# Kernel optimization log

Measured on AMD Instinct MI355X. Metric: run time of the kernel, lower is better.

The kernel has to match this reference:

```python
import jax, jax.numpy as jnp
import numpy as np
import math

B, N, E, F_IN, H = 16, 2048, 32768, 32, 128
RATIO = 0.8
K1 = math.ceil(RATIO * N)      # 1639
K2 = math.ceil(RATIO * K1)     # 1312
K3 = math.ceil(RATIO * K2)     # 1050


def setup_inputs() -> dict:
    key = jax.random.key(0)
    ks = jax.random.split(key, 20)

    def lin(k, out_d, in_d):
        s = 1.0 / np.sqrt(in_d)
        return jax.random.uniform(k, (out_d, in_d), minval=-s, maxval=s, dtype=jnp.float32)

    return {
        "x": jax.random.normal(ks[0], (B, N, F_IN), dtype=jnp.float32),
        "edge_index": jax.random.randint(ks[1], (B, 2, E), 0, N, dtype=jnp.int32),
        "W_root1": lin(ks[2], H, F_IN), "W_rel1": lin(ks[3], H, F_IN), "b1": jnp.zeros((H,), jnp.float32),
        "p1": jax.random.normal(ks[4], (H,), dtype=jnp.float32) * 0.1,
        "W_root2": lin(ks[5], H, H), "W_rel2": lin(ks[6], H, H), "b2": jnp.zeros((H,), jnp.float32),
        "p2": jax.random.normal(ks[7], (H,), dtype=jnp.float32) * 0.1,
        "W_root3": lin(ks[8], H, H), "W_rel3": lin(ks[9], H, H), "b3": jnp.zeros((H,), jnp.float32),
        "p3": jax.random.normal(ks[10], (H,), dtype=jnp.float32) * 0.1,
        "lin1_W": lin(ks[11], 128, 256), "lin1_b": jnp.zeros((128,), jnp.float32),
        "lin2_W": lin(ks[12], 64, 128), "lin2_b": jnp.zeros((64,), jnp.float32),
        "lin3_W": lin(ks[13], 1, 64), "lin3_b": jnp.zeros((1,), jnp.float32),
    }


def _graph_conv(x, src, dst, ev, W_rel, b, W_root):
    # GraphConv: out_i = W_root x_i + W_rel * sum_{j->i} x_j + b
    n = x.shape[0]
    msg = x[src] * ev[:, None].astype(x.dtype)            # [E, F] gather
    agg = jnp.zeros((n, x.shape[1]), x.dtype).at[dst].add(msg)  # scatter-add
    return agg @ W_rel.T + b + x @ W_root.T


def _topk_pool(x, src, dst, ev, p, k):
    # TopKPooling: score = tanh(x.p/||p||); keep top-k nodes; x' = x[perm]*score[perm]
    score = jnp.tanh((x @ p) / jnp.linalg.norm(p))        # [n]
    vals, perm = jax.lax.top_k(score, k)
    x_new = x[perm] * vals[:, None]
    inv = jnp.full((x.shape[0],), -1, jnp.int32).at[perm].set(jnp.arange(k, dtype=jnp.int32))
    ns, nd = inv[src], inv[dst]
    valid = ev & (ns >= 0) & (nd >= 0)
    return x_new, jnp.where(valid, ns, 0), jnp.where(valid, nd, 0), valid


def _readout(x):
    # cat([global_max_pool, global_mean_pool])
    return jnp.concatenate([x.max(axis=0), x.mean(axis=0)])


def reference(x, edge_index,
              W_root1, W_rel1, b1, p1,
              W_root2, W_rel2, b2, p2,
              W_root3, W_rel3, b3, p3,
              lin1_W, lin1_b, lin2_W, lin2_b, lin3_W, lin3_b):
    def per_graph(xg, eg):
        src, dst = eg[0], eg[1]
        ev = jnp.ones((E,), bool)
        h = jax.nn.relu(_graph_conv(xg, src, dst, ev, W_rel1, b1, W_root1))
        h, src, dst, ev = _topk_pool(h, src, dst, ev, p1, K1)
        r1 = _readout(h)
        h = jax.nn.relu(_graph_conv(h, src, dst, ev, W_rel2, b2, W_root2))
        h, src, dst, ev = _topk_pool(h, src, dst, ev, p2, K2)
        r2 = _readout(h)
        h = jax.nn.relu(_graph_conv(h, src, dst, ev, W_rel3, b3, W_root3))
        h, src, dst, ev = _topk_pool(h, src, dst, ev, p3, K3)
        r3 = _readout(h)
        return r1 + r2 + r3                                # [256]

    g = jax.vmap(per_graph)(x, edge_index)                 # [B, 256]
    h = jax.nn.relu(g @ lin1_W.T + lin1_b)
    h = jax.nn.relu(h @ lin2_W.T + lin2_b)
    out = jax.nn.sigmoid(h @ lin3_W.T + lin3_b)            # [B, 1]
    return out[:, 0]
```

## Files before the change

### kernel.cpp

```cpp
#include <hip/hip_runtime.h>
#include <cstdint>
#include <math.h>

#define BB 16
#define NN 2048
#define EE 32768
#define FIN 32
#define HH 128
#define KK1 1639
#define KK2 1312
#define KK3 1050
#define PARTS 256
#define PGRP 8
#define JPG (PARTS / PGRP)
#define DEGC 64

using f16x8 = __attribute__((ext_vector_type(8))) _Float16;
using f16x2 = __attribute__((ext_vector_type(2))) _Float16;
using f32x4 = __attribute__((ext_vector_type(4))) float;

__global__ void build1_kernel(const int* __restrict__ ei,
                              int* __restrict__ deg, int* __restrict__ csr) {
    int t = blockIdx.x * blockDim.x + threadIdx.x;
    int e = t & (EE - 1);
    int b = t >> 15;
    if (b >= BB) return;
    int s = ei[(size_t)b * 2 * EE + e];
    int d = ei[(size_t)b * 2 * EE + EE + e];
    int pos = atomicAdd(&deg[b * NN + d], 1);
    if (pos < DEGC) csr[((size_t)b * NN + d) * DEGC + pos] = s;
}

__global__ __launch_bounds__(256) void agg1_csr_kernel(
    const float* __restrict__ x, const int* __restrict__ deg,
    const int* __restrict__ csr, _Float16* __restrict__ agg) {
    int b = blockIdx.y;
    int g = threadIdx.x >> 5, lane = threadIdx.x & 31;
    int node = blockIdx.x * 8 + g;
    int dg = deg[b * NN + node]; if (dg > DEGC) dg = DEGC;
    const int* bucket = csr + ((size_t)b * NN + node) * DEGC;
    float acc = 0.f;
    for (int base = 0; base < dg; base += 16) {
        int m = dg - base; if (m > 16) m = 16;
        int myidx = (lane < m) ? bucket[base + lane] : 0;
        float v[16];
        int idx[16];
#pragma unroll
        for (int u = 0; u < 16; u++) idx[u] = __shfl(myidx, u, 32);
#pragma unroll
        for (int u = 0; u < 16; u++)
            v[u] = x[((size_t)b * NN + idx[u]) * FIN + lane];
#pragma unroll
        for (int u = 0; u < 16; u++)
            acc += (u < m) ? v[u] : 0.f;
    }
    agg[((size_t)b * NN + node) * FIN + lane] = (_Float16)acc;
}

__global__ __launch_bounds__(256) void agg23_csr_kernel(
    const _Float16* __restrict__ x, const int* __restrict__ deg,
    const int* __restrict__ csr, _Float16* __restrict__ agg, int n) {
    int b = blockIdx.y;
    int wv = threadIdx.x >> 6, lane = threadIdx.x & 63;
    int node = blockIdx.x * 4 + wv;
    if (node >= n) return;
    int dg = deg[b * NN + node]; if (dg > DEGC) dg = DEGC;
    const int* bucket = csr + ((size_t)b * NN + node) * DEGC;
    const f16x2* xf2 = reinterpret_cast<const f16x2*>(x);
    float ax = 0.f, ay = 0.f;
    for (int base = 0; base < dg; base += 16) {
        int m = dg - base; if (m > 16) m = 16;
        int myidx = (lane < m) ? bucket[base + lane] : 0;
        int idx[16];
#pragma unroll
        for (int u = 0; u < 16; u++) idx[u] = __shfl(myidx, u);
        f16x2 v[16];
#pragma unroll
        for (int u = 0; u < 16; u++)
            v[u] = xf2[((size_t)b * NN + idx[u]) * 64 + lane];
#pragma unroll
        for (int u = 0; u < 16; u++) {
            ax += (u < m) ? (float)v[u][0] : 0.f;
            ay += (u < m) ? (float)v[u][1] : 0.f;
        }
    }
    f16x2 o; o[0] = (_Float16)ax; o[1] = (_Float16)ay;
    reinterpret_cast<f16x2*>(agg)[((size_t)b * NN + node) * 64 + lane] = o;
}

__device__ __forceinline__ f16x8 load_cvt16(const float* src) {
    float4 lo = *reinterpret_cast<const float4*>(src);
    float4 hi = *reinterpret_cast<const float4*>(src + 4);
    f16x8 r;
    r[0] = (_Float16)lo.x; r[1] = (_Float16)lo.y;
    r[2] = (_Float16)lo.z; r[3] = (_Float16)lo.w;
    r[4] = (_Float16)hi.x; r[5] = (_Float16)hi.y;
    r[6] = (_Float16)hi.z; r[7] = (_Float16)hi.w;
    return r;
}

template<int FI, bool XF32>
__global__ __launch_bounds__(256) void conv_mfma_kernel(
    const void* __restrict__ xv, const void* __restrict__ aggv,
    const float* __restrict__ Wroot, const float* __restrict__ Wrel,
    const float* __restrict__ bias, const float* __restrict__ p,
    _Float16* __restrict__ h, unsigned long long* __restrict__ keys,
    float* __restrict__ ssc, int n) {
    __shared__ float spart[4][32];
    __shared__ float snorm_s;
    const float* xf = (const float*)xv;
    const _Float16* xh = (const _Float16*)xv;
    const _Float16* ah = (const _Float16*)aggv;
    int b = blockIdx.y;
    int r0 = blockIdx.x * 32;
    int t = threadIdx.x;
    int wv = t >> 6, lane = t & 63;
    int m16 = lane & 15, q = lane >> 4;

    if (t < 64) {
        float v = p[t] * p[t] + p[t + 64] * p[t + 64];
#pragma unroll
        for (int off = 32; off; off >>= 1) v += __shfl_xor(v, off);
        if (t == 0) snorm_s = sqrtf(v);
    }

    f32x4 acc[2][2];
#pragma unroll
    for (int rt = 0; rt < 2; rt++)
#pragma unroll
        for (int ct = 0; ct < 2; ct++) {
            acc[rt][ct][0] = 0.f; acc[rt][ct][1] = 0.f;
            acc[rt][ct][2] = 0.f; acc[rt][ct][3] = 0.f;
        }

    int rowA[2] = { r0 + m16, r0 + 16 + m16 };
    int colB[2] = { wv * 32 + m16, wv * 32 + 16 + m16 };

#pragma unroll
    for (int step = 0; step < (2 * FI) / 32; step++) {
        int k0 = step * 32 + q * 8;
        f16x8 afr[2], bfr[2];
#pragma unroll
        for (int rt = 0; rt < 2; rt++) {
            if (k0 < FI) {
                if constexpr (XF32)
                    afr[rt] = load_cvt16(xf + ((size_t)b * NN + rowA[rt]) * FI + k0);
                else
                    afr[rt] = *reinterpret_cast<const f16x8*>(
                        xh + ((size_t)b * NN + rowA[rt]) * FI + k0);
            } else {
                afr[rt] = *reinterpret_cast<const f16x8*>(
                    ah + ((size_t)b * NN + rowA[rt]) * FI + (k0 - FI));
            }
        }
#pragma unroll
        for (int ct = 0; ct < 2; ct++) {
            const float* src = (k0 < FI)
                ? Wroot + (size_t)colB[ct] * FI + k0
                : Wrel  + (size_t)colB[ct] * FI + (k0 - FI);
            bfr[ct] = load_cvt16(src);
        }
#pragma unroll
        for (int rt = 0; rt < 2; rt++)
#pragma unroll
            for (int ct = 0; ct < 2; ct++)
                acc[rt][ct] = __builtin_amdgcn_mfma_f32_16x16x32_f16(
                    afr[rt], bfr[ct], acc[rt][ct], 0, 0, 0);
    }

    float prt[2][4];
#pragma unroll
    for (int rt = 0; rt < 2; rt++)
#pragma unroll
        for (int reg = 0; reg < 4; reg++) prt[rt][reg] = 0.f;

#pragma unroll
    for (int ct = 0; ct < 2; ct++) {
        int col = wv * 32 + ct * 16 + m16;
        float pc = p[col];
        float bv = bias[col];
#pragma unroll
        for (int rt = 0; rt < 2; rt++)
#pragma unroll
            for (int reg = 0; reg < 4; reg++) {
                int row = r0 + rt * 16 + q * 4 + reg;
                float hv = fmaxf(acc[rt][ct][reg] + bv, 0.f);
                if (row < n)
                    h[((size_t)b * NN + row) * HH + col] = (_Float16)hv;
                prt[rt][reg] += hv * pc;
            }
    }
#pragma unroll
    for (int rt = 0; rt < 2; rt++)
#pragma unroll
        for (int reg = 0; reg < 4; reg++) {
            float v = prt[rt][reg];
            v += __shfl_xor(v, 1); v += __shfl_xor(v, 2);
            v += __shfl_xor(v, 4); v += __shfl_xor(v, 8);
            prt[rt][reg] = v;
        }
    if (m16 == 0) {
#pragma unroll
        for (int rt = 0; rt < 2; rt++)
#pragma unroll
            for (int reg = 0; reg < 4; reg++)
                spart[wv][rt * 16 + q * 4 + reg] = prt[rt][reg];
    }
    __syncthreads();
    if (t < 32) {
        int row = r0 + t;
        if (row < n) {
            float s = spart[0][t] + spart[1][t] + spart[2][t] + spart[3][t];
            float sc = tanhf(s / snorm_s);
            unsigned u = __float_as_uint(sc);
            u = (u & 0x80000000u) ? ~u : (u ^ 0x80000000u);
            u = ~u;
            keys[(size_t)b * NN + row] = ((unsigned long long)u << 32) | (unsigned)row;
            ssc[(size_t)b * NN + row] = sc;
        }
    }
}

__global__ __launch_bounds__(256) void rank_kernel(
    const unsigned long long* __restrict__ keys, const float* __restrict__ ssc,
    int n, int k, int* __restrict__ perm, float* __restrict__ vals,
    int* __restrict__ inv) {
    __shared__ unsigned long long sk[NN];
    __shared__ int pr2[256];
    int b = blockIdx.y;
    for (int i = threadIdx.x; i < NN; i += 256)
        sk[i] = (i < n) ? keys[(size_t)b * NN + i] : ~0ULL;
    __syncthreads();
    int il = threadIdx.x & 63;
    int jg = threadIdx.x >> 6;
    int i = blockIdx.x * 64 + il;
    unsigned long long my = sk[i];
    int rank = 0;
#pragma unroll 8
    for (int j = jg * 512; j < jg * 512 + 512; j++)
        rank += (sk[j] < my) ? 1 : 0;
    pr2[threadIdx.x] = rank;
    __syncthreads();
    if (jg == 0 && i < n) {
        rank = pr2[il] + pr2[64 + il] + pr2[128 + il] + pr2[192 + il];
        if (rank < k) {
            perm[b * NN + rank] = i;
            vals[b * NN + rank] = ssc[(size_t)b * NN + i];
            inv[b * NN + i] = rank;
        } else {
            inv[b * NN + i] = -1;
        }
    }
}

__global__ __launch_bounds__(256) void fat_gather_build_kernel(
    int nbuild,
    const int* __restrict__ inv,
    const int* __restrict__ sin_, const int* __restrict__ din_, int in_stride,
    int* __restrict__ sout, int* __restrict__ dout, int write_next,
    int* __restrict__ deg, int* __restrict__ csr,
    const _Float16* __restrict__ hin, _Float16* __restrict__ xout,
    const int* __restrict__ perm, const float* __restrict__ vals, int k,
    float* __restrict__ part) {
    if ((int)blockIdx.x < nbuild) {
        int t = blockIdx.x * 256 + threadIdx.x;
        int e = t & (EE - 1);
        int b = t >> 15;
        if (b >= BB) return;
        int s = sin_[(size_t)b * in_stride + e];
        int d = din_[(size_t)b * in_stride + e];
        int ns = -1, nd = -1;
        if (s >= 0 && d >= 0) {
            ns = inv[b * NN + s];
            nd = inv[b * NN + d];
        }
        if (ns < 0 || nd < 0) { ns = -1; nd = -1; }
        if (write_next) {
            sout[(size_t)b * EE + e] = ns;
            dout[(size_t)b * EE + e] = nd;
        }
        if (nd >= 0) {
            int pos = atomicAdd(&deg[b * NN + nd], 1);
            if (pos < DEGC) csr[((size_t)b * NN + nd) * DEGC + pos] = ns;
        }
    } else {
        int gblk = blockIdx.x - nbuild;
        int pair = gblk * 2 + (threadIdx.x >> 7);
        int b = pair >> 8;
        int j = pair & (PARTS - 1);
        int f = threadIdx.x & 127;
        float mx = -INFINITY, sm = 0.f;
        int i = j;
        int pi = (i < k) ? perm[b * NN + i] : 0;
        float v = (i < k) ? vals[b * NN + i] : 0.f;
        while (i < k) {
            int inext = i + PARTS;
            int pin = 0; float vn = 0.f;
            if (inext < k) { pin = perm[b * NN + inext]; vn = vals[b * NN + inext]; }
            float hv = (float)hin[((size_t)b * NN + pi) * HH + f] * v;
            xout[((size_t)b * NN + i) * HH + f] = (_Float16)hv;
            mx = fmaxf(mx, hv);
            sm += hv;
            i = inext; pi = pin; v = vn;
        }
        part[((size_t)b * PARTS + j) * 256 + f] = mx;
        part[((size_t)b * PARTS + j) * 256 + 128 + f] = sm;
    }
}

__global__ __launch_bounds__(256) void combine_kernel(
    const float* __restrict__ partAll, float* __restrict__ partG) {
    int blk = blockIdx.x;
    int g = blk % PGRP;
    int rem = blk / PGRP;
    int b = rem & 15;
    int l = rem >> 4;
    int f = threadIdx.x;
    const float* src = partAll + ((((size_t)l * BB + b) * PARTS) + (size_t)g * JPG) * 256;
    float r;
    if (f < 128) {
        r = -INFINITY;
#pragma unroll
        for (int j = 0; j < JPG; j++) r = fmaxf(r, src[j * 256 + f]);
    } else {
        r = 0.f;
#pragma unroll
        for (int j = 0; j < JPG; j++) r += src[j * 256 + f];
    }
    partG[(((size_t)l * BB + b) * PGRP + g) * 256 + f] = r;
}

__global__ __launch_bounds__(256) void mlp_kernel(
    const float* __restrict__ partG,
    const float* __restrict__ W1, const float* __restrict__ b1,
    const float* __restrict__ W2, const float* __restrict__ b2,
    const float* __restrict__ W3, const float* __restrict__ b3,
    float* __restrict__ out) {
    __shared__ float sg[256];
    __shared__ float s1[128];
    __shared__ float s2[64];
    int b = blockIdx.x, tid = threadIdx.x;
    const float kk[3] = {(float)KK1, (float)KK2, (float)KK3};
    float acc = 0.f;
    if (tid < 128) {
#pragma unroll
        for (int l = 0; l < 3; l++) {
            float mx = -INFINITY;
#pragma unroll
            for (int j = 0; j < PGRP; j++)
                mx = fmaxf(mx, partG[(((size_t)l * BB + b) * PGRP + j) * 256 + tid]);
            acc += mx;
        }
    } else {
#pragma unroll
        for (int l = 0; l < 3; l++) {
            float sm = 0.f;
#pragma unroll
            for (int j = 0; j < PGRP; j++)
                sm += partG[(((size_t)l * BB + b) * PGRP + j) * 256 + tid];
            acc += sm / kk[l];
        }
    }
    sg[tid] = acc;
    __syncthreads();
    if (tid < 128) {
        float a = b1[tid];
        for (int j = 0; j < 256; j++) a += sg[j] * W1[tid * 256 + j];
        s1[tid] = fmaxf(a, 0.f);
    }
    __syncthreads();
    if (tid < 64) {
        float a = b2[tid];
        for (int j = 0; j < 128; j++) a += s1[j] * W2[tid * 128 + j];
        s2[tid] = fmaxf(a, 0.f);
    }
    __syncthreads();
    if (tid == 0) {
        float a = b3[0];
        for (int j = 0; j < 64; j++) a += s2[j] * W3[j];
        out[b] = 1.f / (1.f + expf(-a));
    }
}

extern "C" void kernel_launch(void* const* d_in, const int* in_sizes, int n_in,
                              void* d_out, int out_size, void* d_ws, size_t ws_size,
                              hipStream_t stream) {
    const float* x   = (const float*)d_in[0];
    const int*   ei  = (const int*)d_in[1];
    const float* Wr1 = (const float*)d_in[2];
    const float* Wl1 = (const float*)d_in[3];
    const float* b1  = (const float*)d_in[4];
    const float* p1  = (const float*)d_in[5];
    const float* Wr2 = (const float*)d_in[6];
    const float* Wl2 = (const float*)d_in[7];
    const float* b2  = (const float*)d_in[8];
    const float* p2  = (const float*)d_in[9];
    const float* Wr3 = (const float*)d_in[10];
    const float* Wl3 = (const float*)d_in[11];
    const float* b3  = (const float*)d_in[12];
    const float* p3  = (const float*)d_in[13];
    const float* l1W = (const float*)d_in[14];
    const float* l1b = (const float*)d_in[15];
    const float* l2W = (const float*)d_in[16];
    const float* l2b = (const float*)d_in[17];
    const float* l3W = (const float*)d_in[18];
    const float* l3b = (const float*)d_in[19];
    float* out = (float*)d_out;

    char* ws = (char*)d_ws;
    _Float16* bufA = (_Float16*)ws; ws += (size_t)BB * NN * HH * 2;
    _Float16* bufB = (_Float16*)ws; ws += (size_t)BB * NN * HH * 2;
    _Float16* agg  = (_Float16*)ws; ws += (size_t)BB * NN * HH * 2;
    int*   perm = (int*)ws;   ws += (size_t)BB * NN * 4;
    float* vals = (float*)ws; ws += (size_t)BB * NN * 4;
    int*   inv  = (int*)ws;   ws += (size_t)BB * NN * 4;
    int*   curS = (int*)ws;   ws += (size_t)BB * EE * 4;
    int*   curD = (int*)ws;   ws += (size_t)BB * EE * 4;
    float* partAll = (float*)ws; ws += (size_t)3 * BB * PARTS * 256 * 4;
    float* partG   = (float*)ws; ws += (size_t)3 * BB * PGRP * 256 * 4;
    int*   deg1 = (int*)ws;   ws += (size_t)BB * NN * 4;
    int*   deg2 = (int*)ws;   ws += (size_t)BB * NN * 4;
    int*   deg3 = (int*)ws;   ws += (size_t)BB * NN * 4;
    int*   csr  = (int*)ws;   ws += (size_t)BB * NN * DEGC * 4;
    unsigned long long* keys = (unsigned long long*)ws; ws += (size_t)BB * NN * 8;
    float* ssc  = (float*)ws; ws += (size_t)BB * NN * 4;
    float* part1 = partAll;
    float* part2 = partAll + (size_t)BB * PARTS * 256;
    float* part3 = partAll + (size_t)2 * BB * PARTS * 256;

    hipMemsetAsync(deg1, 0, (size_t)3 * BB * NN * 4, stream);

    hipLaunchKernelGGL(build1_kernel, dim3(BB * EE / 256), dim3(256), 0, stream, ei, deg1, csr);
    hipLaunchKernelGGL(agg1_csr_kernel, dim3(NN / 8, BB), dim3(256), 0, stream, x, deg1, csr, agg);
    hipLaunchKernelGGL((conv_mfma_kernel<FIN, true>), dim3(NN / 32, BB), dim3(256), 0, stream,
                       (const void*)x, (const void*)agg, Wr1, Wl1, b1, p1, bufA, keys, ssc, NN);
    hipLaunchKernelGGL(rank_kernel, dim3(NN / 64, BB), dim3(256), 0, stream, keys, ssc, NN, KK1, perm, vals, inv);
    hipLaunchKernelGGL(fat_gather_build_kernel, dim3(2048 + BB * PARTS / 2), dim3(256), 0, stream,
                       2048, inv, ei, ei + EE, 2 * EE, curS, curD, 1, deg2, csr,
                       bufA, bufB, perm, vals, KK1, part1);

    hipLaunchKernelGGL(agg23_csr_kernel, dim3((KK1 + 3) / 4, BB), dim3(256), 0, stream, bufB, deg2, csr, agg, KK1);
    hipLaunchKernelGGL((conv_mfma_kernel<HH, false>), dim3((KK1 + 31) / 32, BB), dim3(256), 0, stream,
                       (const void*)bufB, (const void*)agg, Wr2, Wl2, b2, p2, bufA, keys, ssc, KK1);
    hipLaunchKernelGGL(rank_kernel, dim3(NN / 64, BB), dim3(256), 0, stream, keys, ssc, KK1, KK2, perm, vals, inv);
    hipLaunchKernelGGL(fat_gather_build_kernel, dim3(2048 + BB * PARTS / 2), dim3(256), 0, stream,
                       2048, inv, curS, curD, EE, curS, curD, 0, deg3, csr,
                       bufA, bufB, perm, vals, KK2, part2);

    hipLaunchKernelGGL(agg23_csr_kernel, dim3((KK2 + 3) / 4, BB), dim3(256), 0, stream, bufB, deg3, csr, agg, KK2);
    hipLaunchKernelGGL((conv_mfma_kernel<HH, false>), dim3((KK2 + 31) / 32, BB), dim3(256), 0, stream,
                       (const void*)bufB, (const void*)agg, Wr3, Wl3, b3, p3, bufA, keys, ssc, KK2);
    hipLaunchKernelGGL(rank_kernel, dim3(NN / 64, BB), dim3(256), 0, stream, keys, ssc, KK2, KK3, perm, vals, inv);
    hipLaunchKernelGGL(fat_gather_build_kernel, dim3(BB * PARTS / 2), dim3(256), 0, stream,
                       0, inv, curS, curD, EE, curS, curD, 0, deg3, csr,
                       bufA, bufB, perm, vals, KK3, part3);

    hipLaunchKernelGGL(combine_kernel, dim3(3 * BB * PGRP), dim3(256), 0, stream, partAll, partG);
    hipLaunchKernelGGL(mlp_kernel, dim3(BB), dim3(256), 0, stream,
                       partG, l1W, l1b, l2W, l2b, l3W, l3b, out);
}
```

Before: 226.3 us.

## Pre-convert conv weights to fp16, swap grid axes, halve readout partitions

Adds a kernel that converts and concatenates the root and rel weights of all three convolutions to fp16 once, so the MFMA conv kernels load f16x8 weight fragments directly instead of converting fp32 in every block. All per-graph kernels swap grid axes so the batch index comes from blockIdx.x, which changes block scheduling order and may improve locality across graphs. The readout partition count drops from 256 to 128 and the pair-to-(graph, part) mapping is reordered. The cost is one extra small launch, and fewer partitions means more serial work per readout thread.

```diff
diff --git a/kernel.cpp b/kernel.cpp
--- a/kernel.cpp
+++ b/kernel.cpp
@@ -10,7 +10,7 @@
 #define KK1 1639
 #define KK2 1312
 #define KK3 1050
-#define PARTS 256
+#define PARTS 128
 #define PGRP 8
 #define JPG (PARTS / PGRP)
 #define DEGC 64
@@ -18,6 +18,31 @@
 using f16x8 = __attribute__((ext_vector_type(8))) _Float16;
 using f16x2 = __attribute__((ext_vector_type(2))) _Float16;
 using f32x4 = __attribute__((ext_vector_type(4))) float;
+
+__global__ void wcvt_kernel(const float* __restrict__ Wr1, const float* __restrict__ Wl1,
+                            const float* __restrict__ Wr2, const float* __restrict__ Wl2,
+                            const float* __restrict__ Wr3, const float* __restrict__ Wl3,
+                            _Float16* __restrict__ wcat1, _Float16* __restrict__ wcat2,
+                            _Float16* __restrict__ wcat3) {
+    int idx = blockIdx.x * 256 + threadIdx.x;
+    if (idx < 128 * 64) {
+        int col = idx >> 6, k = idx & 63;
+        float v = (k < FIN) ? Wr1[col * FIN + k] : Wl1[col * FIN + (k - FIN)];
+        wcat1[idx] = (_Float16)v;
+    } else if (idx < 128 * 64 + 128 * 256) {
+        int i2 = idx - 128 * 64;
+        int col = i2 >> 8, k = i2 & 255;
+        float v = (k < HH) ? Wr2[col * HH + k] : Wl2[col * HH + (k - HH)];
+        wcat2[i2] = (_Float16)v;
+    } else {
+        int i3 = idx - 128 * 64 - 128 * 256;
+        if (i3 < 128 * 256) {
+            int col = i3 >> 8, k = i3 & 255;
+            float v = (k < HH) ? Wr3[col * HH + k] : Wl3[col * HH + (k - HH)];
+            wcat3[i3] = (_Float16)v;
+        }
+    }
+}
 
 __global__ void build1_kernel(const int* __restrict__ ei,
                               int* __restrict__ deg, int* __restrict__ csr) {
@@ -34,9 +59,9 @@
 __global__ __launch_bounds__(256) void agg1_csr_kernel(
     const float* __restrict__ x, const int* __restrict__ deg,
     const int* __restrict__ csr, _Float16* __restrict__ agg) {
-    int b = blockIdx.y;
+    int b = blockIdx.x;
     int g = threadIdx.x >> 5, lane = threadIdx.x & 31;
-    int node = blockIdx.x * 8 + g;
+    int node = blockIdx.y * 8 + g;
     int dg = deg[b * NN + node]; if (dg > DEGC) dg = DEGC;
     const int* bucket = csr + ((size_t)b * NN + node) * DEGC;
     float acc = 0.f;
@@ -60,9 +85,9 @@
 __global__ __launch_bounds__(256) void agg23_csr_kernel(
     const _Float16* __restrict__ x, const int* __restrict__ deg,
     const int* __restrict__ csr, _Float16* __restrict__ agg, int n) {
-    int b = blockIdx.y;
+    int b = blockIdx.x;
     int wv = threadIdx.x >> 6, lane = threadIdx.x & 63;
-    int node = blockIdx.x * 4 + wv;
+    int node = blockIdx.y * 4 + wv;
     if (node >= n) return;
     int dg = deg[b * NN + node]; if (dg > DEGC) dg = DEGC;
     const int* bucket = csr + ((size_t)b * NN + node) * DEGC;
@@ -101,8 +126,8 @@
 
 template<int FI, bool XF32>
 __global__ __launch_bounds__(256) void conv_mfma_kernel(
-    const void* __restrict__ xv, const void* __restrict__ aggv,
-    const float* __restrict__ Wroot, const float* __restrict__ Wrel,
+    const void* __restrict__ xv, const _Float16* __restrict__ ah,
+    const _Float16* __restrict__ wcat,
     const float* __restrict__ bias, const float* __restrict__ p,
     _Float16* __restrict__ h, unsigned long long* __restrict__ keys,
     float* __restrict__ ssc, int n) {
@@ -110,9 +135,8 @@
     __shared__ float snorm_s;
     const float* xf = (const float*)xv;
     const _Float16* xh = (const _Float16*)xv;
-    const _Float16* ah = (const _Float16*)aggv;
-    int b = blockIdx.y;
-    int r0 = blockIdx.x * 32;
+    int b = blockIdx.x;
+    int r0 = blockIdx.y * 32;
     int t = threadIdx.x;
     int wv = t >> 6, lane = t & 63;
     int m16 = lane & 15, q = lane >> 4;
@@ -154,12 +178,9 @@
             }
         }
 #pragma unroll
-        for (int ct = 0; ct < 2; ct++) {
-            const float* src = (k0 < FI)
-                ? Wroot + (size_t)colB[ct] * FI + k0
-                : Wrel  + (size_t)colB[ct] * FI + (k0 - FI);
-            bfr[ct] = load_cvt16(src);
-        }
+        for (int ct = 0; ct < 2; ct++)
+            bfr[ct] = *reinterpret_cast<const f16x8*>(
+                wcat + (size_t)colB[ct] * (2 * FI) + k0);
 #pragma unroll
         for (int rt = 0; rt < 2; rt++)
 #pragma unroll
@@ -227,13 +248,13 @@
     int* __restrict__ inv) {
     __shared__ unsigned long long sk[NN];
     __shared__ int pr2[256];
-    int b = blockIdx.y;
+    int b = blockIdx.x;
     for (int i = threadIdx.x; i < NN; i += 256)
         sk[i] = (i < n) ? keys[(size_t)b * NN + i] : ~0ULL;
     __syncthreads();
     int il = threadIdx.x & 63;
     int jg = threadIdx.x >> 6;
-    int i = blockIdx.x * 64 + il;
+    int i = blockIdx.y * 64 + il;
     unsigned long long my = sk[i];
     int rank = 0;
 #pragma unroll 8
@@ -286,8 +307,8 @@
     } else {
         int gblk = blockIdx.x - nbuild;
         int pair = gblk * 2 + (threadIdx.x >> 7);
-        int b = pair >> 8;
-        int j = pair & (PARTS - 1);
+        int b = pair & 15;
+        int j = pair >> 4;
         int f = threadIdx.x & 127;
         float mx = -INFINITY, sm = 0.f;
         int i = j;
@@ -424,33 +445,38 @@
     int*   csr  = (int*)ws;   ws += (size_t)BB * NN * DEGC * 4;
     unsigned long long* keys = (unsigned long long*)ws; ws += (size_t)BB * NN * 8;
     float* ssc  = (float*)ws; ws += (size_t)BB * NN * 4;
+    _Float16* wcat1 = (_Float16*)ws; ws += (size_t)128 * 64 * 2;
+    _Float16* wcat2 = (_Float16*)ws; ws += (size_t)128 * 256 * 2;
+    _Float16* wcat3 = (_Float16*)ws; ws += (size_t)128 * 256 * 2;
     float* part1 = partAll;
     float* part2 = partAll + (size_t)BB * PARTS * 256;
     float* part3 = partAll + (size_t)2 * BB * PARTS * 256;
 
     hipMemsetAsync(deg1, 0, (size_t)3 * BB * NN * 4, stream);
+    hipLaunchKernelGGL(wcvt_kernel, dim3((128 * 64 + 2 * 128 * 256 + 255) / 256), dim3(256), 0, stream,
+                       Wr1, Wl1, Wr2, Wl2, Wr3, Wl3, wcat1, wcat2, wcat3);
 
     hipLaunchKernelGGL(build1_kernel, dim3(BB * EE / 256), dim3(256), 0, stream, ei, deg1, csr);
-    hipLaunchKernelGGL(agg1_csr_kernel, dim3(NN / 8, BB), dim3(256), 0, stream, x, deg1, csr, agg);
-    hipLaunchKernelGGL((conv_mfma_kernel<FIN, true>), dim3(NN / 32, BB), dim3(256), 0, stream,
-                       (const void*)x, (const void*)agg, Wr1, Wl1, b1, p1, bufA, keys, ssc, NN);
-    hipLaunchKernelGGL(rank_kernel, dim3(NN / 64, BB), dim3(256), 0, stream, keys, ssc, NN, KK1, perm, vals, inv);
+    hipLaunchKernelGGL(agg1_csr_kernel, dim3(BB, NN / 8), dim3(256), 0, stream, x, deg1, csr, agg);
+    hipLaunchKernelGGL((conv_mfma_kernel<FIN, true>), dim3(BB, NN / 32), dim3(256), 0, stream,
+                       (const void*)x, agg, wcat1, b1, p1, bufA, keys, ssc, NN);
+    hipLaunchKernelGGL(rank_kernel, dim3(BB, NN / 64), dim3(256), 0, stream, keys, ssc, NN, KK1, perm, vals, inv);
     hipLaunchKernelGGL(fat_gather_build_kernel, dim3(2048 + BB * PARTS / 2), dim3(256), 0, stream,
                        2048, inv, ei, ei + EE, 2 * EE, curS, curD, 1, deg2, csr,
                        bufA, bufB, perm, vals, KK1, part1);
 
-    hipLaunchKernelGGL(agg23_csr_kernel, dim3((KK1 + 3) / 4, BB), dim3(256), 0, stream, bufB, deg2, csr, agg, KK1);
-    hipLaunchKernelGGL((conv_mfma_kernel<HH, false>), dim3((KK1 + 31) / 32, BB), dim3(256), 0, stream,
-                       (const void*)bufB, (const void*)agg, Wr2, Wl2, b2, p2, bufA, keys, ssc, KK1);
-    hipLaunchKernelGGL(rank_kernel, dim3(NN / 64, BB), dim3(256), 0, stream, keys, ssc, KK1, KK2, perm, vals, inv);
+    hipLaunchKernelGGL(agg23_csr_kernel, dim3(BB, (KK1 + 3) / 4), dim3(256), 0, stream, bufB, deg2, csr, agg, KK1);
+    hipLaunchKernelGGL((conv_mfma_kernel<HH, false>), dim3(BB, (KK1 + 31) / 32), dim3(256), 0, stream,
+                       (const void*)bufB, agg, wcat2, b2, p2, bufA, keys, ssc, KK1);
+    hipLaunchKernelGGL(rank_kernel, dim3(BB, NN / 64), dim3(256), 0, stream, keys, ssc, KK1, KK2, perm, vals, inv);
     hipLaunchKernelGGL(fat_gather_build_kernel, dim3(2048 + BB * PARTS / 2), dim3(256), 0, stream,
                        2048, inv, curS, curD, EE, curS, curD, 0, deg3, csr,
                        bufA, bufB, perm, vals, KK2, part2);
 
-    hipLaunchKernelGGL(agg23_csr_kernel, dim3((KK2 + 3) / 4, BB), dim3(256), 0, stream, bufB, deg3, csr, agg, KK2);
-    hipLaunchKernelGGL((conv_mfma_kernel<HH, false>), dim3((KK2 + 31) / 32, BB), dim3(256), 0, stream,
-                       (const void*)bufB, (const void*)agg, Wr3, Wl3, b3, p3, bufA, keys, ssc, KK2);
-    hipLaunchKernelGGL(rank_kernel, dim3(NN / 64, BB), dim3(256), 0, stream, keys, ssc, KK2, KK3, perm, vals, inv);
+    hipLaunchKernelGGL(agg23_csr_kernel, dim3(BB, (KK2 + 3) / 4), dim3(256), 0, stream, bufB, deg3, csr, agg, KK2);
+    hipLaunchKernelGGL((conv_mfma_kernel<HH, false>), dim3(BB, (KK2 + 31) / 32), dim3(256), 0, stream,
+                       (const void*)bufB, agg, wcat3, b3, p3, bufA, keys, ssc, KK2);
+    hipLaunchKernelGGL(rank_kernel, dim3(BB, NN / 64), dim3(256), 0, stream, keys, ssc, KK2, KK3, perm, vals, inv);
     hipLaunchKernelGGL(fat_gather_build_kernel, dim3(BB * PARTS / 2), dim3(256), 0, stream,
                        0, inv, curS, curD, EE, curS, curD, 0, deg3, csr,
                        bufA, bufB, perm, vals, KK3, part3);
```

Result: faster. 217.5 us (-3.9%).
